# Kernel tuning notes

Measured on AMD Instinct MI355X. Metric: run time of the kernel, lower is better.

## Reference

```python
import jax, jax.numpy as jnp
import numpy as np


def _gcn_layer(x, row, col, W, b, num_nodes):
    # Linear projection then scatter-add aggregation: out[col] += h[row].
    # NOTE: the original module computes a symmetric degree norm but its
    # message() returns x_j unscaled, so aggregation is a plain (unnormalized)
    # sum -- we reproduce that faithfully.
    h = x @ W.T + b                      # [N, out]
    msg = h[row]                          # [E+N, out] gathered source feats
    return jax.ops.segment_sum(msg, col, num_segments=num_nodes)


def setup_inputs() -> dict:
    key = jax.random.key(0)
    k1, k2, k3, k4, k5, k6 = jax.random.split(key, 6)
    N, E = 50000, 600000
    IN, HID, OUT = 128, 128, 64
    x = jax.random.normal(k1, (N, IN), dtype=jnp.float32)
    edge_index = jax.random.randint(k2, (2, E), 0, N, dtype=jnp.int64)
    s1 = 1.0 / np.sqrt(IN)
    s2 = 1.0 / np.sqrt(HID)
    W1 = jax.random.uniform(k3, (HID, IN), jnp.float32, -s1, s1)
    b1 = jax.random.uniform(k4, (HID,), jnp.float32, -s1, s1)
    W2 = jax.random.uniform(k5, (OUT, HID), jnp.float32, -s2, s2)
    b2 = jax.random.uniform(k6, (OUT,), jnp.float32, -s2, s2)
    return {"x": x, "edge_index": edge_index, "W1": W1, "b1": b1, "W2": W2, "b2": b2}


def reference(x, edge_index, W1, b1, W2, b2):
    N = x.shape[0]
    loops = jnp.arange(N, dtype=edge_index.dtype)
    row = jnp.concatenate([edge_index[0], loops])
    col = jnp.concatenate([edge_index[1], loops])
    h = _gcn_layer(x, row, col, W1, b1, N)
    h = jax.nn.relu(h)  # dropout is identity in eval mode
    h = _gcn_layer(h, row, col, W2, b2, N)
    return jax.nn.log_softmax(h, axis=1)
```

## Files before the change

### kernel.cpp

```cpp
#include <hip/hip_runtime.h>


#define K4 32

template <int F, int CT, bool RELU_IN>
__global__ __launch_bounds__(256, 2) void gemm_kernel(
    const float* __restrict__ X, const float* __restrict__ W,
    const float* __restrict__ bias, float* __restrict__ H, int M) {
  constexpr int RT = 8;
  constexpr int TM = 128;
  __shared__ float4 wlds[F * K4];

  const int tid = threadIdx.x;

  {
    const float4* W4 = reinterpret_cast<const float4*>(W);
#pragma unroll
    for (int it = 0; it < F * K4 / 256; ++it) {
      const int f = it * 256 + tid;
      const int c = f >> 5;
      const int qs = f & 31;
      wlds[f] = W4[c * K4 + (qs ^ ((c >> 3) & 7))];
    }
  }
  __syncthreads();

  const int cg = tid & 15;
  const int rg = tid >> 4;
  const int c0 = cg * CT;
  const int m0 = blockIdx.x * TM + rg * RT;

  int rbase[RT];
#pragma unroll
  for (int i = 0; i < RT; ++i) rbase[i] = min(m0 + i, M - 1) * K4;
  const int wswz = (c0 >> 3) & 7;
  const float4* wrow = &wlds[c0 * K4];

  const float4* X4 = reinterpret_cast<const float4*>(X);

  float acc[RT][CT];
#pragma unroll
  for (int i = 0; i < RT; ++i)
#pragma unroll
    for (int j = 0; j < CT; ++j) acc[i][j] = 0.f;

#pragma unroll 2
  for (int q = 0; q < K4; ++q) {
    float4 a[RT];
#pragma unroll
    for (int i = 0; i < RT; ++i) {
      float4 v = X4[rbase[i] + q];
      if (RELU_IN) {
        v.x = fmaxf(v.x, 0.f); v.y = fmaxf(v.y, 0.f);
        v.z = fmaxf(v.z, 0.f); v.w = fmaxf(v.w, 0.f);
      }
      a[i] = v;
    }
    const int qs = q ^ wswz;
    float4 wv[CT];
#pragma unroll
    for (int j = 0; j < CT; ++j) wv[j] = wrow[j * K4 + qs];
#pragma unroll
    for (int i = 0; i < RT; ++i)
#pragma unroll
      for (int j = 0; j < CT; ++j)
        acc[i][j] += a[i].x * wv[j].x + a[i].y * wv[j].y +
                     a[i].z * wv[j].z + a[i].w * wv[j].w;
  }

  float bj[CT];
#pragma unroll
  for (int j = 0; j < CT; ++j) bj[j] = bias[c0 + j];
  float4* H4 = reinterpret_cast<float4*>(H);
#pragma unroll
  for (int i = 0; i < RT; ++i) {
    const int m = m0 + i;
    if (m < M) {
#pragma unroll
      for (int jc = 0; jc < CT / 4; ++jc) {
        float4 o;
        o.x = acc[i][jc * 4 + 0] + bj[jc * 4 + 0];
        o.y = acc[i][jc * 4 + 1] + bj[jc * 4 + 1];
        o.z = acc[i][jc * 4 + 2] + bj[jc * 4 + 2];
        o.w = acc[i][jc * 4 + 3] + bj[jc * 4 + 3];
        H4[(size_t)m * (F / 4) + (c0 >> 2) + jc] = o;
      }
    }
  }
}

__global__ __launch_bounds__(256) void zero_kernel(int* __restrict__ p, int n) {
  const int i = blockIdx.x * 256 + threadIdx.x;
  if (i < n) p[i] = 0;
}

__global__ __launch_bounds__(256) void fill_kernel(
    const int* __restrict__ rows, const int* __restrict__ cols,
    int* __restrict__ cnt, int* __restrict__ srcs, int E) {
  const int e = blockIdx.x * 256 + threadIdx.x;
  if (e >= E) return;
  const int c = cols[e];
  const int pos = atomicAdd(&cnt[c], 1);
  if (pos < 64) srcs[(c << 6) + pos] = rows[e];
}

__global__ __launch_bounds__(256) void gather128_kernel(
    const int* __restrict__ cnt, const int* __restrict__ srcs,
    const float* __restrict__ H, float* __restrict__ AGG, int N) {
  const int node = blockIdx.x * 8 + (threadIdx.x >> 5);
  if (node >= N) return;
  const int lane = threadIdx.x & 31;
  const int n = min(cnt[node], 64);
  const int base = node << 6;
  const float4* H4 = reinterpret_cast<const float4*>(H);
  float4 acc = H4[(size_t)node * 32 + lane];
  int j = 0;
  for (; j + 4 <= n; j += 4) {
    const int4 s = *reinterpret_cast<const int4*>(&srcs[base + j]);
    const float4 v0 = H4[(size_t)s.x * 32 + lane];
    const float4 v1 = H4[(size_t)s.y * 32 + lane];
    const float4 v2 = H4[(size_t)s.z * 32 + lane];
    const float4 v3 = H4[(size_t)s.w * 32 + lane];
    acc.x += (v0.x + v1.x) + (v2.x + v3.x);
    acc.y += (v0.y + v1.y) + (v2.y + v3.y);
    acc.z += (v0.z + v1.z) + (v2.z + v3.z);
    acc.w += (v0.w + v1.w) + (v2.w + v3.w);
  }
  for (; j < n; ++j) {
    const float4 v = H4[(size_t)srcs[base + j] * 32 + lane];
    acc.x += v.x; acc.y += v.y; acc.z += v.z; acc.w += v.w;
  }
  reinterpret_cast<float4*>(AGG)[(size_t)node * 32 + lane] = acc;
}

__global__ __launch_bounds__(256) void gather64_lsm_kernel(
    const int* __restrict__ cnt, const int* __restrict__ srcs,
    const float* __restrict__ H, float* __restrict__ OUT, int N) {
  const int node = blockIdx.x * 16 + (threadIdx.x >> 4);
  if (node >= N) return;
  const int lane = threadIdx.x & 15;
  const int n = min(cnt[node], 64);
  const int base = node << 6;
  const float4* H4 = reinterpret_cast<const float4*>(H);
  float4 acc = H4[(size_t)node * 16 + lane];
  int j = 0;
  for (; j + 4 <= n; j += 4) {
    const int4 s = *reinterpret_cast<const int4*>(&srcs[base + j]);
    const float4 v0 = H4[(size_t)s.x * 16 + lane];
    const float4 v1 = H4[(size_t)s.y * 16 + lane];
    const float4 v2 = H4[(size_t)s.z * 16 + lane];
    const float4 v3 = H4[(size_t)s.w * 16 + lane];
    acc.x += (v0.x + v1.x) + (v2.x + v3.x);
    acc.y += (v0.y + v1.y) + (v2.y + v3.y);
    acc.z += (v0.z + v1.z) + (v2.z + v3.z);
    acc.w += (v0.w + v1.w) + (v2.w + v3.w);
  }
  for (; j < n; ++j) {
    const float4 v = H4[(size_t)srcs[base + j] * 16 + lane];
    acc.x += v.x; acc.y += v.y; acc.z += v.z; acc.w += v.w;
  }
  float mx = fmaxf(fmaxf(acc.x, acc.y), fmaxf(acc.z, acc.w));
#pragma unroll
  for (int s = 8; s > 0; s >>= 1) mx = fmaxf(mx, __shfl_xor(mx, s));
  float sum = __expf(acc.x - mx) + __expf(acc.y - mx) +
              __expf(acc.z - mx) + __expf(acc.w - mx);
#pragma unroll
  for (int s = 8; s > 0; s >>= 1) sum += __shfl_xor(sum, s);
  const float lse = mx + __logf(sum);
  float4 o;
  o.x = acc.x - lse; o.y = acc.y - lse; o.z = acc.z - lse; o.w = acc.w - lse;
  reinterpret_cast<float4*>(OUT)[(size_t)node * 16 + lane] = o;
}

extern "C" void kernel_launch(void* const* d_in, const int* in_sizes, int n_in,
                              void* d_out, int out_size, void* d_ws,
                              size_t ws_size, hipStream_t stream) {
  const float* x  = (const float*)d_in[0];
  const int* ei   = (const int*)d_in[1];
  const float* W1 = (const float*)d_in[2];
  const float* b1 = (const float*)d_in[3];
  const float* W2 = (const float*)d_in[4];
  const float* b2 = (const float*)d_in[5];
  float* out = (float*)d_out;

  const int N = in_sizes[0] / 128;
  const int E = in_sizes[1] / 2;
  const int* rows = ei;
  const int* cols = ei + E;

  float* h1   = (float*)d_ws;
  float* agg1 = h1 + (size_t)N * 128;
  float* h2   = h1;
  int* cnt    = (int*)(agg1 + (size_t)N * 128);
  int* srcs   = cnt + N;

  zero_kernel<<<(N + 255) / 256, 256, 0, stream>>>(cnt, N);
  fill_kernel<<<(E + 255) / 256, 256, 0, stream>>>(rows, cols, cnt, srcs, E);

  gemm_kernel<128, 8, false>
      <<<(N + 127) / 128, 256, 0, stream>>>(x, W1, b1, h1, N);
  gather128_kernel<<<(N + 7) / 8, 256, 0, stream>>>(cnt, srcs, h1, agg1, N);

  gemm_kernel<64, 4, true>
      <<<(N + 127) / 128, 256, 0, stream>>>(agg1, W2, b2, h2, N);
  gather64_lsm_kernel<<<(N + 15) / 16, 256, 0, stream>>>(cnt, srcs, h2, out, N);
}
```

Measured before the change: 256.9 us.

## Split GEMM output columns across grid y and double-buffer X loads

```diff
diff --git a/kernel.cpp b/kernel.cpp
--- a/kernel.cpp
+++ b/kernel.cpp
@@ -3,24 +3,25 @@
 
 #define K4 32
 
-template <int F, int CT, bool RELU_IN>
-__global__ __launch_bounds__(256, 2) void gemm_kernel(
+template <int F, int FB, int CT, bool RELU_IN>
+__global__ __launch_bounds__(256, 4) void gemm_kernel(
     const float* __restrict__ X, const float* __restrict__ W,
     const float* __restrict__ bias, float* __restrict__ H, int M) {
   constexpr int RT = 8;
   constexpr int TM = 128;
-  __shared__ float4 wlds[F * K4];
+  __shared__ float4 wlds[FB * K4];
 
   const int tid = threadIdx.x;
+  const int foff = blockIdx.y * FB;
 
   {
     const float4* W4 = reinterpret_cast<const float4*>(W);
 #pragma unroll
-    for (int it = 0; it < F * K4 / 256; ++it) {
+    for (int it = 0; it < FB * K4 / 256; ++it) {
       const int f = it * 256 + tid;
-      const int c = f >> 5;
+      const int cl = f >> 5;
       const int qs = f & 31;
-      wlds[f] = W4[c * K4 + (qs ^ ((c >> 3) & 7))];
+      wlds[f] = W4[(foff + cl) * K4 + (qs ^ ((cl >> 3) & 7))];
     }
   }
   __syncthreads();
@@ -44,47 +45,68 @@
 #pragma unroll
     for (int j = 0; j < CT; ++j) acc[i][j] = 0.f;
 
-#pragma unroll 2
-  for (int q = 0; q < K4; ++q) {
-    float4 a[RT];
-#pragma unroll
-    for (int i = 0; i < RT; ++i) {
-      float4 v = X4[rbase[i] + q];
-      if (RELU_IN) {
-        v.x = fmaxf(v.x, 0.f); v.y = fmaxf(v.y, 0.f);
-        v.z = fmaxf(v.z, 0.f); v.w = fmaxf(v.w, 0.f);
+  float4 aP[RT], aQ[RT];
+#pragma unroll
+  for (int i = 0; i < RT; ++i) aP[i] = X4[rbase[i]];
+
+  for (int qq = 0; qq < K4; qq += 2) {
+#pragma unroll
+    for (int i = 0; i < RT; ++i) aQ[i] = X4[rbase[i] + qq + 1];
+    {
+      const int qs = qq ^ wswz;
+      float4 wv[CT];
+#pragma unroll
+      for (int j = 0; j < CT; ++j) wv[j] = wrow[j * K4 + qs];
+#pragma unroll
+      for (int i = 0; i < RT; ++i) {
+        float4 v = aP[i];
+        if (RELU_IN) {
+          v.x = fmaxf(v.x, 0.f); v.y = fmaxf(v.y, 0.f);
+          v.z = fmaxf(v.z, 0.f); v.w = fmaxf(v.w, 0.f);
+        }
+#pragma unroll
+        for (int j = 0; j < CT; ++j)
+          acc[i][j] += v.x * wv[j].x + v.y * wv[j].y +
+                       v.z * wv[j].z + v.w * wv[j].w;
       }
-      a[i] = v;
-    }
-    const int qs = q ^ wswz;
-    float4 wv[CT];
-#pragma unroll
-    for (int j = 0; j < CT; ++j) wv[j] = wrow[j * K4 + qs];
-#pragma unroll
-    for (int i = 0; i < RT; ++i)
-#pragma unroll
-      for (int j = 0; j < CT; ++j)
-        acc[i][j] += a[i].x * wv[j].x + a[i].y * wv[j].y +
-                     a[i].z * wv[j].z + a[i].w * wv[j].w;
+    }
+    const int qn = min(qq + 2, K4 - 1);
+#pragma unroll
+    for (int i = 0; i < RT; ++i) aP[i] = X4[rbase[i] + qn];
+    {
+      const int qs = (qq + 1) ^ wswz;
+      float4 wv[CT];
+#pragma unroll
+      for (int j = 0; j < CT; ++j) wv[j] = wrow[j * K4 + qs];
+#pragma unroll
+      for (int i = 0; i < RT; ++i) {
+        float4 v = aQ[i];
+        if (RELU_IN) {
+          v.x = fmaxf(v.x, 0.f); v.y = fmaxf(v.y, 0.f);
+          v.z = fmaxf(v.z, 0.f); v.w = fmaxf(v.w, 0.f);
+        }
+#pragma unroll
+        for (int j = 0; j < CT; ++j)
+          acc[i][j] += v.x * wv[j].x + v.y * wv[j].y +
+                       v.z * wv[j].z + v.w * wv[j].w;
+      }
+    }
   }
 
   float bj[CT];
 #pragma unroll
-  for (int j = 0; j < CT; ++j) bj[j] = bias[c0 + j];
+  for (int j = 0; j < CT; ++j) bj[j] = bias[foff + c0 + j];
   float4* H4 = reinterpret_cast<float4*>(H);
 #pragma unroll
   for (int i = 0; i < RT; ++i) {
     const int m = m0 + i;
     if (m < M) {
-#pragma unroll
-      for (int jc = 0; jc < CT / 4; ++jc) {
-        float4 o;
-        o.x = acc[i][jc * 4 + 0] + bj[jc * 4 + 0];
-        o.y = acc[i][jc * 4 + 1] + bj[jc * 4 + 1];
-        o.z = acc[i][jc * 4 + 2] + bj[jc * 4 + 2];
-        o.w = acc[i][jc * 4 + 3] + bj[jc * 4 + 3];
-        H4[(size_t)m * (F / 4) + (c0 >> 2) + jc] = o;
-      }
+      float4 o;
+      o.x = acc[i][0] + bj[0];
+      o.y = acc[i][1] + bj[1];
+      o.z = acc[i][2] + bj[2];
+      o.w = acc[i][3] + bj[3];
+      H4[(size_t)m * (F / 4) + ((foff + c0) >> 2)] = o;
     }
   }
 }
@@ -197,11 +219,11 @@
   zero_kernel<<<(N + 255) / 256, 256, 0, stream>>>(cnt, N);
   fill_kernel<<<(E + 255) / 256, 256, 0, stream>>>(rows, cols, cnt, srcs, E);
 
-  gemm_kernel<128, 8, false>
-      <<<(N + 127) / 128, 256, 0, stream>>>(x, W1, b1, h1, N);
+  gemm_kernel<128, 64, 4, false>
+      <<<dim3((N + 127) / 128, 2), 256, 0, stream>>>(x, W1, b1, h1, N);
   gather128_kernel<<<(N + 7) / 8, 256, 0, stream>>>(cnt, srcs, h1, agg1, N);
 
-  gemm_kernel<64, 4, true>
-      <<<(N + 127) / 128, 256, 0, stream>>>(agg1, W2, b2, h2, N);
+  gemm_kernel<64, 64, 4, true>
+      <<<dim3((N + 127) / 128, 1), 256, 0, stream>>>(agg1, W2, b2, h2, N);
   gather64_lsm_kernel<<<(N + 15) / 16, 256, 0, stream>>>(cnt, srcs, h2, out, N);
 }
```

After: 621.7 us. +142.0%, slower.
